# Optimization experiments

Measured on AMD Instinct MI355X. Metric: run time of the kernel, lower is better.

The kernel has to match this reference:

```python
import jax, jax.numpy as jnp
import numpy as np

BLOCK = 64  # block_len

def segsum(x):
    # x: (..., T) -> (..., T, T) lower-triangular segment sums, -inf above diagonal
    T = x.shape[-1]
    cs = jnp.cumsum(x, axis=-1)
    seg = cs[..., :, None] - cs[..., None, :]
    mask = jnp.tril(jnp.ones((T, T), dtype=bool))
    return jnp.where(mask, seg, -jnp.inf)

def setup_inputs() -> dict:
    key = jax.random.key(0)
    k1, k2, k3, k4 = jax.random.split(key, 4)
    b, T, h, p, n = 2, 4096, 32, 64, 64
    X  = jax.random.normal(k1, (b, T, h, p), dtype=jnp.float32)
    # decay rates: negative, bounded, for numerical stability of exp(segsum)
    A  = -0.5 * jax.random.uniform(k2, (b, T, h), dtype=jnp.float32)
    Bm = jax.random.normal(k3, (b, T, h, n), dtype=jnp.float32)
    Cm = jax.random.normal(k4, (b, T, h, n), dtype=jnp.float32)
    return {"X": X, "A": A, "Bm": Bm, "Cm": Cm}

def reference(X, A, Bm, Cm):
    b, T, h, p = X.shape
    n = Bm.shape[-1]
    l = BLOCK
    c = T // l
    # chunk into blocks: b (c l) ... -> b c l ...
    Xb = X.reshape(b, c, l, h, p)
    Bb = Bm.reshape(b, c, l, h, n)
    Cb = Cm.reshape(b, c, l, h, n)
    Ab = A.reshape(b, c, l, h).transpose(0, 3, 1, 2)  # b h c l
    A_cs = jnp.cumsum(Ab, axis=-1)                    # b h c l
    # 1. intra-chunk (diagonal block) output
    L = jnp.exp(segsum(Ab))                           # b h c l l
    Y_diag = jnp.einsum('bclhn,bcshn,bhcls,bcshp->bclhp', Cb, Bb, L, Xb)
    # 2. per-chunk final states
    decay_states = jnp.exp(A_cs[:, :, :, -1:] - A_cs)  # b h c l
    states = jnp.einsum('bclhn,bhcl,bclhp->bchpn', Bb, decay_states, Xb)
    # 3. inter-chunk recurrence (initial state = 0)
    states = jnp.concatenate([jnp.zeros_like(states[:, :1]), states], axis=1)  # b (c+1) h p n
    chunk_sums = jnp.pad(A_cs[:, :, :, -1], ((0, 0), (0, 0), (1, 0)))          # b h (c+1)
    decay_chunk = jnp.exp(segsum(chunk_sums))                                  # b h (c+1) (c+1)
    new_states = jnp.einsum('bhzc,bchpn->bzhpn', decay_chunk, states)[:, :-1]  # b c h p n
    # 4. state -> output (off-diagonal blocks)
    state_decay_out = jnp.exp(A_cs)                                            # b h c l
    Y_off = jnp.einsum('bclhn,bchpn,bhcl->bclhp', Cb, new_states, state_decay_out)
    return (Y_diag + Y_off).reshape(b, T, h, p)
```

## Files before the change

### kernel.cpp

```cpp
#include <hip/hip_runtime.h>
#include <cstddef>

#define NB 2
#define T_ 4096
#define H_ 32
#define P_ 64
#define N_ 64
#define L_ 64
#define C_ 64
#define LDB 72

typedef __attribute__((ext_vector_type(8))) short short8;
typedef __attribute__((ext_vector_type(4))) short short4v;
typedef __attribute__((ext_vector_type(4))) float f32x4;

static __device__ inline short f2bf(float f) {
    unsigned u = __builtin_bit_cast(unsigned, f);
    u += 0x7fffu + ((u >> 16) & 1u);
    return (short)(u >> 16);
}

static __device__ inline short8 ldfrag(const short* s, int t16, int kt, int lane) {
    return *(const short8*)(s + (t16 * 16 + (lane & 15)) * LDB + kt * 32 + ((lane >> 4) * 8));
}

__global__ __launch_bounds__(256) void k1_states(
    const float* __restrict__ X, const float* __restrict__ A,
    const float* __restrict__ Bm, float* __restrict__ St, float* __restrict__ tot)
{
    __shared__ short sXt[L_ * LDB];
    __shared__ short sBt[L_ * LDB];
    __shared__ float sAcs[L_];

    const int tid = threadIdx.x, lane = tid & 63, wv = tid >> 6;
    const int idx = blockIdx.x;
    const int h  = idx & (H_ - 1);
    const int c  = (idx >> 5) & (C_ - 1);
    const int bb = idx >> 11;
    const int t0 = c * L_;

    if (wv == 0) {
        float v = A[(size_t)(bb * T_ + t0 + lane) * H_ + h];
        #pragma unroll
        for (int d = 1; d < 64; d <<= 1) {
            float o = __shfl_up(v, (unsigned)d);
            if (lane >= d) v += o;
        }
        sAcs[lane] = v;
        if (lane == 63) tot[(bb * H_ + h) * C_ + c] = v;
    }
    __syncthreads();
    const float totv = sAcs[L_ - 1];

    const int bi = tid >> 4, bp = tid & 15;
    const int i0 = bi * 4, p0 = bp * 4;
    float4 xr[4], br[4];
    #pragma unroll
    for (int k = 0; k < 4; k++) {
        const size_t g = ((size_t)(bb * T_ + t0 + i0 + k) * H_ + h) * P_ + p0;
        xr[k] = *(const float4*)(X + g);
        br[k] = *(const float4*)(Bm + g);
    }
    float dec[4];
    #pragma unroll
    for (int k = 0; k < 4; k++) dec[k] = expf(totv - sAcs[i0 + k]);
    #pragma unroll
    for (int j = 0; j < 4; j++) {
        short4v vx, vb;
        #pragma unroll
        for (int k = 0; k < 4; k++) {
            vx[k] = f2bf(((const float*)&xr[k])[j]);
            vb[k] = f2bf(((const float*)&br[k])[j] * dec[k]);
        }
        *(short4v*)&sXt[(p0 + j) * LDB + i0] = vx;
        *(short4v*)&sBt[(p0 + j) * LDB + i0] = vb;
    }
    __syncthreads();

    const short8 a0 = ldfrag(sXt, wv, 0, lane);
    const short8 a1 = ldfrag(sXt, wv, 1, lane);
    const size_t sbase = ((size_t)((bb * C_ + c) * H_ + h)) * (N_ * P_);
    const int prow = wv * 16 + (lane >> 4) * 4;
    const int ncol = lane & 15;
    #pragma unroll
    for (int nt = 0; nt < 4; nt++) {
        f32x4 acc = {0.f, 0.f, 0.f, 0.f};
        acc = __builtin_amdgcn_mfma_f32_16x16x32_bf16(a0, ldfrag(sBt, nt, 0, lane), acc, 0, 0, 0);
        acc = __builtin_amdgcn_mfma_f32_16x16x32_bf16(a1, ldfrag(sBt, nt, 1, lane), acc, 0, 0, 0);
        #pragma unroll
        for (int r = 0; r < 4; r++)
            St[sbase + (size_t)(prow + r) * N_ + nt * 16 + ncol] = acc[r];
    }
}

__global__ __launch_bounds__(256) void k2_scan(
    float* __restrict__ St, const float* __restrict__ tot)
{
    const int idx = blockIdx.x;
    const int split = idx & 7;
    const int h  = (idx >> 3) & (H_ - 1);
    const int bb = idx >> 8;
    const int e  = split * 512 + threadIdx.x;
    const float* tp = &tot[(bb * H_ + h) * C_];

    float c0 = 0.f, c1 = 0.f;
    for (int c = 0; c < C_; c++) {
        const float d = expf(tp[c]);
        const size_t base = ((size_t)((bb * C_ + c) * H_ + h)) * (N_ * P_);
        const float t0v = St[base + e];
        const float t1v = St[base + e + 256];
        St[base + e]       = c0;
        St[base + e + 256] = c1;
        c0 = c0 * d + t0v;
        c1 = c1 * d + t1v;
    }
}

__global__ __launch_bounds__(256) void k3_out(
    const float* __restrict__ X, const float* __restrict__ A,
    const float* __restrict__ Bm, const float* __restrict__ Cm,
    const float* __restrict__ St, float* __restrict__ Y)
{
    __shared__ short sC [L_ * LDB];
    __shared__ short sB [L_ * LDB];
    __shared__ short sXt[L_ * LDB];
    __shared__ short sNS[L_ * LDB];
    __shared__ short sS [L_ * LDB];
    __shared__ float sAcs[L_];

    const int tid = threadIdx.x, lane = tid & 63, wv = tid >> 6;
    const int idx = blockIdx.x;
    const int h  = idx & (H_ - 1);
    const int c  = (idx >> 5) & (C_ - 1);
    const int bb = idx >> 11;
    const int t0 = c * L_;
    const size_t sbase = ((size_t)((bb * C_ + c) * H_ + h)) * (N_ * P_);

    if (wv == 0) {
        float v = A[(size_t)(bb * T_ + t0 + lane) * H_ + h];
        #pragma unroll
        for (int d = 1; d < 64; d <<= 1) {
            float o = __shfl_up(v, (unsigned)d);
            if (lane >= d) v += o;
        }
        sAcs[lane] = v;
    }

    #pragma unroll
    for (int f = tid; f < L_ * 16; f += 256) {
        const int row = f >> 4, c4 = (f & 15) << 2;
        const size_t g = ((size_t)(bb * T_ + t0 + row) * H_ + h) * P_ + c4;
        const float4 vc = *(const float4*)(Cm + g);
        const float4 vb = *(const float4*)(Bm + g);
        const float4 vs = *(const float4*)(St + sbase + (size_t)row * N_ + c4);
        short4v c2, b2, s2;
        #pragma unroll
        for (int k = 0; k < 4; k++) {
            c2[k] = f2bf(((const float*)&vc)[k]);
            b2[k] = f2bf(((const float*)&vb)[k]);
            s2[k] = f2bf(((const float*)&vs)[k]);
        }
        *(short4v*)&sC [row * LDB + c4] = c2;
        *(short4v*)&sB [row * LDB + c4] = b2;
        *(short4v*)&sNS[row * LDB + c4] = s2;
    }
    {
        const int bi = tid >> 4, bp = tid & 15;
        const int i0 = bi * 4, p0 = bp * 4;
        float4 xr[4];
        #pragma unroll
        for (int k = 0; k < 4; k++) {
            const size_t g = ((size_t)(bb * T_ + t0 + i0 + k) * H_ + h) * P_ + p0;
            xr[k] = *(const float4*)(X + g);
        }
        #pragma unroll
        for (int j = 0; j < 4; j++) {
            short4v vx;
            #pragma unroll
            for (int k = 0; k < 4; k++) vx[k] = f2bf(((const float*)&xr[k])[j]);
            *(short4v*)&sXt[(p0 + j) * LDB + i0] = vx;
        }
    }
    __syncthreads();

    const short8 c0f = ldfrag(sC, wv, 0, lane);
    const short8 c1f = ldfrag(sC, wv, 1, lane);
    const int rbase = wv * 16 + (lane >> 4) * 4;
    const int col   = lane & 15;

    f32x4 accO[4];
    #pragma unroll
    for (int pt = 0; pt < 4; pt++) {
        f32x4 a = {0.f, 0.f, 0.f, 0.f};
        a = __builtin_amdgcn_mfma_f32_16x16x32_bf16(c0f, ldfrag(sNS, pt, 0, lane), a, 0, 0, 0);
        a = __builtin_amdgcn_mfma_f32_16x16x32_bf16(c1f, ldfrag(sNS, pt, 1, lane), a, 0, 0, 0);
        accO[pt] = a;
    }

    float csr[4];
    #pragma unroll
    for (int r = 0; r < 4; r++) csr[r] = sAcs[rbase + r];
    #pragma unroll
    for (int st = 0; st < 4; st++) {
        f32x4 a = {0.f, 0.f, 0.f, 0.f};
        a = __builtin_amdgcn_mfma_f32_16x16x32_bf16(c0f, ldfrag(sB, st, 0, lane), a, 0, 0, 0);
        a = __builtin_amdgcn_mfma_f32_16x16x32_bf16(c1f, ldfrag(sB, st, 1, lane), a, 0, 0, 0);
        const int scol = st * 16 + col;
        const float ccs = sAcs[scol];
        #pragma unroll
        for (int r = 0; r < 4; r++) {
            const float v = (scol <= rbase + r) ? a[r] * expf(csr[r] - ccs) : 0.f;
            sS[(rbase + r) * LDB + scol] = f2bf(v);
        }
    }

    const short8 s0f = ldfrag(sS, wv, 0, lane);
    const short8 s1f = ldfrag(sS, wv, 1, lane);
    float exr[4];
    #pragma unroll
    for (int r = 0; r < 4; r++) exr[r] = expf(csr[r]);
    #pragma unroll
    for (int pt = 0; pt < 4; pt++) {
        f32x4 a = {0.f, 0.f, 0.f, 0.f};
        a = __builtin_amdgcn_mfma_f32_16x16x32_bf16(s0f, ldfrag(sXt, pt, 0, lane), a, 0, 0, 0);
        a = __builtin_amdgcn_mfma_f32_16x16x32_bf16(s1f, ldfrag(sXt, pt, 1, lane), a, 0, 0, 0);
        #pragma unroll
        for (int r = 0; r < 4; r++) {
            const size_t g = ((size_t)(bb * T_ + t0 + rbase + r) * H_ + h) * P_ + pt * 16 + col;
            Y[g] = a[r] + exr[r] * accO[pt][r];
        }
    }
}

extern "C" void kernel_launch(void* const* d_in, const int* in_sizes, int n_in,
                              void* d_out, int out_size, void* d_ws, size_t ws_size,
                              hipStream_t stream)
{
    const float* X  = (const float*)d_in[0];
    const float* A  = (const float*)d_in[1];
    const float* Bm = (const float*)d_in[2];
    const float* Cm = (const float*)d_in[3];
    float* Y   = (float*)d_out;
    float* St  = (float*)d_ws;
    float* tot = St + (size_t)NB * C_ * H_ * N_ * P_;

    k1_states<<<NB * C_ * H_, 256, 0, stream>>>(X, A, Bm, St, tot);
    k2_scan  <<<NB * H_ * 8, 256, 0, stream>>>(St, tot);
    k3_out   <<<NB * C_ * H_, 256, 0, stream>>>(X, A, Bm, Cm, St, Y);
}
```

Measured before the change: 279.3 us.

## Fuse state, scan and output kernels into one sequential-chunk kernel with register carry

Replaces the three-kernel pipeline (per-chunk states, global scan over chunk states, output) with one kernel per (batch, head, 16-column P slice). Each block walks the 64 chunks in order, keeps the running state in registers, and prefetches the next chunk's inputs into registers while computing the current one. This removes the round-trip of the full state tensor through global memory and two kernel launches. The cost is only 256 blocks of serial 64-step work, which lowers parallelism, and the C·Bᵀ intra-chunk product is now recomputed by each of the four P-slice blocks.

```diff
diff --git a/kernel.cpp b/kernel.cpp
--- a/kernel.cpp
+++ b/kernel.cpp
@@ -24,211 +24,169 @@
     return *(const short8*)(s + (t16 * 16 + (lane & 15)) * LDB + kt * 32 + ((lane >> 4) * 8));
 }
 
-__global__ __launch_bounds__(256) void k1_states(
+__global__ __launch_bounds__(256) void fused_ssd(
     const float* __restrict__ X, const float* __restrict__ A,
-    const float* __restrict__ Bm, float* __restrict__ St, float* __restrict__ tot)
+    const float* __restrict__ Bm, const float* __restrict__ Cm,
+    float* __restrict__ Y)
 {
-    __shared__ short sXt[L_ * LDB];
+    __shared__ short sC [L_ * LDB];
+    __shared__ short sB [L_ * LDB];
     __shared__ short sBt[L_ * LDB];
-    __shared__ float sAcs[L_];
+    __shared__ short sS [L_ * LDB];
+    __shared__ short sXt[16 * LDB];
+    __shared__ short sNS[16 * LDB];
+    __shared__ float sAcs[2][L_];
 
     const int tid = threadIdx.x, lane = tid & 63, wv = tid >> 6;
     const int idx = blockIdx.x;
-    const int h  = idx & (H_ - 1);
-    const int c  = (idx >> 5) & (C_ - 1);
-    const int bb = idx >> 11;
-    const int t0 = c * L_;
-
+    const int q  = idx & 3;
+    const int h  = (idx >> 2) & (H_ - 1);
+    const int bb = idx >> 7;
+    const int p0 = q * 16;
+
+    const int bi = tid >> 4, bp = tid & 15;
+    const int xrow = tid >> 2, xpq = tid & 3;
+
+    float4 rC[4], rB[4], rX;
+    float rA;
+    f32x4 carry = {0.f, 0.f, 0.f, 0.f};
+
+    #pragma unroll
+    for (int k = 0; k < 4; k++) {
+        const size_t g = ((size_t)(bb * T_ + 4 * bi + k) * H_ + h) * P_ + 4 * bp;
+        rC[k] = *(const float4*)(Cm + g);
+        rB[k] = *(const float4*)(Bm + g);
+    }
+    rX = *(const float4*)(X + ((size_t)(bb * T_ + xrow) * H_ + h) * P_ + p0 + 4 * xpq);
+    rA = (tid < 64) ? A[(size_t)(bb * T_ + lane) * H_ + h] : 0.f;
     if (wv == 0) {
-        float v = A[(size_t)(bb * T_ + t0 + lane) * H_ + h];
+        float v = rA;
         #pragma unroll
         for (int d = 1; d < 64; d <<= 1) {
             float o = __shfl_up(v, (unsigned)d);
             if (lane >= d) v += o;
         }
-        sAcs[lane] = v;
-        if (lane == 63) tot[(bb * H_ + h) * C_ + c] = v;
+        sAcs[0][lane] = v;
     }
     __syncthreads();
-    const float totv = sAcs[L_ - 1];
-
-    const int bi = tid >> 4, bp = tid & 15;
-    const int i0 = bi * 4, p0 = bp * 4;
-    float4 xr[4], br[4];
-    #pragma unroll
-    for (int k = 0; k < 4; k++) {
-        const size_t g = ((size_t)(bb * T_ + t0 + i0 + k) * H_ + h) * P_ + p0;
-        xr[k] = *(const float4*)(X + g);
-        br[k] = *(const float4*)(Bm + g);
-    }
-    float dec[4];
-    #pragma unroll
-    for (int k = 0; k < 4; k++) dec[k] = expf(totv - sAcs[i0 + k]);
-    #pragma unroll
-    for (int j = 0; j < 4; j++) {
-        short4v vx, vb;
-        #pragma unroll
-        for (int k = 0; k < 4; k++) {
-            vx[k] = f2bf(((const float*)&xr[k])[j]);
-            vb[k] = f2bf(((const float*)&br[k])[j] * dec[k]);
-        }
-        *(short4v*)&sXt[(p0 + j) * LDB + i0] = vx;
-        *(short4v*)&sBt[(p0 + j) * LDB + i0] = vb;
-    }
-    __syncthreads();
-
-    const short8 a0 = ldfrag(sXt, wv, 0, lane);
-    const short8 a1 = ldfrag(sXt, wv, 1, lane);
-    const size_t sbase = ((size_t)((bb * C_ + c) * H_ + h)) * (N_ * P_);
-    const int prow = wv * 16 + (lane >> 4) * 4;
-    const int ncol = lane & 15;
-    #pragma unroll
-    for (int nt = 0; nt < 4; nt++) {
-        f32x4 acc = {0.f, 0.f, 0.f, 0.f};
-        acc = __builtin_amdgcn_mfma_f32_16x16x32_bf16(a0, ldfrag(sBt, nt, 0, lane), acc, 0, 0, 0);
-        acc = __builtin_amdgcn_mfma_f32_16x16x32_bf16(a1, ldfrag(sBt, nt, 1, lane), acc, 0, 0, 0);
-        #pragma unroll
-        for (int r = 0; r < 4; r++)
-            St[sbase + (size_t)(prow + r) * N_ + nt * 16 + ncol] = acc[r];
-    }
-}
-
-__global__ __launch_bounds__(256) void k2_scan(
-    float* __restrict__ St, const float* __restrict__ tot)
-{
-    const int idx = blockIdx.x;
-    const int split = idx & 7;
-    const int h  = (idx >> 3) & (H_ - 1);
-    const int bb = idx >> 8;
-    const int e  = split * 512 + threadIdx.x;
-    const float* tp = &tot[(bb * H_ + h) * C_];
-
-    float c0 = 0.f, c1 = 0.f;
+
     for (int c = 0; c < C_; c++) {
-        const float d = expf(tp[c]);
-        const size_t base = ((size_t)((bb * C_ + c) * H_ + h)) * (N_ * P_);
-        const float t0v = St[base + e];
-        const float t1v = St[base + e + 256];
-        St[base + e]       = c0;
-        St[base + e + 256] = c1;
-        c0 = c0 * d + t0v;
-        c1 = c1 * d + t1v;
-    }
-}
-
-__global__ __launch_bounds__(256) void k3_out(
-    const float* __restrict__ X, const float* __restrict__ A,
-    const float* __restrict__ Bm, const float* __restrict__ Cm,
-    const float* __restrict__ St, float* __restrict__ Y)
-{
-    __shared__ short sC [L_ * LDB];
-    __shared__ short sB [L_ * LDB];
-    __shared__ short sXt[L_ * LDB];
-    __shared__ short sNS[L_ * LDB];
-    __shared__ short sS [L_ * LDB];
-    __shared__ float sAcs[L_];
-
-    const int tid = threadIdx.x, lane = tid & 63, wv = tid >> 6;
-    const int idx = blockIdx.x;
-    const int h  = idx & (H_ - 1);
-    const int c  = (idx >> 5) & (C_ - 1);
-    const int bb = idx >> 11;
-    const int t0 = c * L_;
-    const size_t sbase = ((size_t)((bb * C_ + c) * H_ + h)) * (N_ * P_);
-
-    if (wv == 0) {
-        float v = A[(size_t)(bb * T_ + t0 + lane) * H_ + h];
-        #pragma unroll
-        for (int d = 1; d < 64; d <<= 1) {
-            float o = __shfl_up(v, (unsigned)d);
-            if (lane >= d) v += o;
-        }
-        sAcs[lane] = v;
-    }
-
-    #pragma unroll
-    for (int f = tid; f < L_ * 16; f += 256) {
-        const int row = f >> 4, c4 = (f & 15) << 2;
-        const size_t g = ((size_t)(bb * T_ + t0 + row) * H_ + h) * P_ + c4;
-        const float4 vc = *(const float4*)(Cm + g);
-        const float4 vb = *(const float4*)(Bm + g);
-        const float4 vs = *(const float4*)(St + sbase + (size_t)row * N_ + c4);
-        short4v c2, b2, s2;
-        #pragma unroll
-        for (int k = 0; k < 4; k++) {
-            c2[k] = f2bf(((const float*)&vc)[k]);
-            b2[k] = f2bf(((const float*)&vb)[k]);
-            s2[k] = f2bf(((const float*)&vs)[k]);
-        }
-        *(short4v*)&sC [row * LDB + c4] = c2;
-        *(short4v*)&sB [row * LDB + c4] = b2;
-        *(short4v*)&sNS[row * LDB + c4] = s2;
-    }
-    {
-        const int bi = tid >> 4, bp = tid & 15;
-        const int i0 = bi * 4, p0 = bp * 4;
-        float4 xr[4];
-        #pragma unroll
-        for (int k = 0; k < 4; k++) {
-            const size_t g = ((size_t)(bb * T_ + t0 + i0 + k) * H_ + h) * P_ + p0;
-            xr[k] = *(const float4*)(X + g);
-        }
-        #pragma unroll
-        for (int j = 0; j < 4; j++) {
-            short4v vx;
-            #pragma unroll
-            for (int k = 0; k < 4; k++) vx[k] = f2bf(((const float*)&xr[k])[j]);
-            *(short4v*)&sXt[(p0 + j) * LDB + i0] = vx;
-        }
-    }
-    __syncthreads();
-
-    const short8 c0f = ldfrag(sC, wv, 0, lane);
-    const short8 c1f = ldfrag(sC, wv, 1, lane);
-    const int rbase = wv * 16 + (lane >> 4) * 4;
-    const int col   = lane & 15;
-
-    f32x4 accO[4];
-    #pragma unroll
-    for (int pt = 0; pt < 4; pt++) {
-        f32x4 a = {0.f, 0.f, 0.f, 0.f};
-        a = __builtin_amdgcn_mfma_f32_16x16x32_bf16(c0f, ldfrag(sNS, pt, 0, lane), a, 0, 0, 0);
-        a = __builtin_amdgcn_mfma_f32_16x16x32_bf16(c1f, ldfrag(sNS, pt, 1, lane), a, 0, 0, 0);
-        accO[pt] = a;
-    }
-
-    float csr[4];
-    #pragma unroll
-    for (int r = 0; r < 4; r++) csr[r] = sAcs[rbase + r];
-    #pragma unroll
-    for (int st = 0; st < 4; st++) {
-        f32x4 a = {0.f, 0.f, 0.f, 0.f};
-        a = __builtin_amdgcn_mfma_f32_16x16x32_bf16(c0f, ldfrag(sB, st, 0, lane), a, 0, 0, 0);
-        a = __builtin_amdgcn_mfma_f32_16x16x32_bf16(c1f, ldfrag(sB, st, 1, lane), a, 0, 0, 0);
-        const int scol = st * 16 + col;
-        const float ccs = sAcs[scol];
+        const int buf = c & 1;
+        const int t0 = c * L_;
+        const float* acs = sAcs[buf];
+
+        {
+            const float totv = acs[L_ - 1];
+            float dec[4];
+            #pragma unroll
+            for (int k = 0; k < 4; k++) dec[k] = expf(totv - acs[4 * bi + k]);
+            #pragma unroll
+            for (int k = 0; k < 4; k++) {
+                short4v vc, vb;
+                #pragma unroll
+                for (int j = 0; j < 4; j++) {
+                    vc[j] = f2bf(((const float*)&rC[k])[j]);
+                    vb[j] = f2bf(((const float*)&rB[k])[j]);
+                }
+                *(short4v*)&sC[(4 * bi + k) * LDB + 4 * bp] = vc;
+                *(short4v*)&sB[(4 * bi + k) * LDB + 4 * bp] = vb;
+            }
+            #pragma unroll
+            for (int j = 0; j < 4; j++) {
+                short4v vt;
+                #pragma unroll
+                for (int k = 0; k < 4; k++)
+                    vt[k] = f2bf(((const float*)&rB[k])[j] * dec[k]);
+                *(short4v*)&sBt[(4 * bp + j) * LDB + 4 * bi] = vt;
+            }
+            #pragma unroll
+            for (int j = 0; j < 4; j++)
+                sXt[(4 * xpq + j) * LDB + xrow] = f2bf(((const float*)&rX)[j]);
+            {
+                const int prow = (lane >> 4) * 4, ncol = wv * 16 + (lane & 15);
+                #pragma unroll
+                for (int r = 0; r < 4; r++)
+                    sNS[(prow + r) * LDB + ncol] = f2bf(carry[r]);
+            }
+        }
+        __syncthreads();
+
+        if (c + 1 < C_) {
+            const int t1 = t0 + L_;
+            #pragma unroll
+            for (int k = 0; k < 4; k++) {
+                const size_t g = ((size_t)(bb * T_ + t1 + 4 * bi + k) * H_ + h) * P_ + 4 * bp;
+                rC[k] = *(const float4*)(Cm + g);
+                rB[k] = *(const float4*)(Bm + g);
+            }
+            rX = *(const float4*)(X + ((size_t)(bb * T_ + t1 + xrow) * H_ + h) * P_ + p0 + 4 * xpq);
+            rA = (tid < 64) ? A[(size_t)(bb * T_ + t1 + lane) * H_ + h] : 0.f;
+        }
+
+        const int rb = (lane >> 4) * 4;
+        const int rbase = wv * 16 + rb;
+        const int col = lane & 15;
+        float csr[4];
+        #pragma unroll
+        for (int r = 0; r < 4; r++) csr[r] = acs[rbase + r];
+        const float totv = acs[L_ - 1];
+
+        const short8 c0f = ldfrag(sC, wv, 0, lane);
+        const short8 c1f = ldfrag(sC, wv, 1, lane);
+
+        f32x4 accY = {0.f, 0.f, 0.f, 0.f};
+        accY = __builtin_amdgcn_mfma_f32_16x16x32_bf16(c0f, ldfrag(sNS, 0, 0, lane), accY, 0, 0, 0);
+        accY = __builtin_amdgcn_mfma_f32_16x16x32_bf16(c1f, ldfrag(sNS, 0, 1, lane), accY, 0, 0, 0);
+        #pragma unroll
+        for (int r = 0; r < 4; r++) accY[r] *= expf(csr[r]);
+
+        #pragma unroll
+        for (int st = 0; st < 4; st++) {
+            f32x4 a = {0.f, 0.f, 0.f, 0.f};
+            a = __builtin_amdgcn_mfma_f32_16x16x32_bf16(c0f, ldfrag(sB, st, 0, lane), a, 0, 0, 0);
+            a = __builtin_amdgcn_mfma_f32_16x16x32_bf16(c1f, ldfrag(sB, st, 1, lane), a, 0, 0, 0);
+            const int scol = st * 16 + col;
+            const float ccs = acs[scol];
+            #pragma unroll
+            for (int r = 0; r < 4; r++) {
+                const float v = (scol <= rbase + r) ? a[r] * expf(csr[r] - ccs) : 0.f;
+                sS[(rbase + r) * LDB + scol] = f2bf(v);
+            }
+        }
+
+        {
+            const short8 s0f = ldfrag(sS, wv, 0, lane);
+            const short8 s1f = ldfrag(sS, wv, 1, lane);
+            accY = __builtin_amdgcn_mfma_f32_16x16x32_bf16(s0f, ldfrag(sXt, 0, 0, lane), accY, 0, 0, 0);
+            accY = __builtin_amdgcn_mfma_f32_16x16x32_bf16(s1f, ldfrag(sXt, 0, 1, lane), accY, 0, 0, 0);
+        }
+
+        {
+            f32x4 stf = {0.f, 0.f, 0.f, 0.f};
+            stf = __builtin_amdgcn_mfma_f32_16x16x32_bf16(ldfrag(sXt, 0, 0, lane), ldfrag(sBt, wv, 0, lane), stf, 0, 0, 0);
+            stf = __builtin_amdgcn_mfma_f32_16x16x32_bf16(ldfrag(sXt, 0, 1, lane), ldfrag(sBt, wv, 1, lane), stf, 0, 0, 0);
+            const float etot = expf(totv);
+            #pragma unroll
+            for (int r = 0; r < 4; r++) carry[r] = carry[r] * etot + stf[r];
+        }
+
+        if (wv == 0 && c + 1 < C_) {
+            float v = rA;
+            #pragma unroll
+            for (int d = 1; d < 64; d <<= 1) {
+                float o = __shfl_up(v, (unsigned)d);
+                if (lane >= d) v += o;
+            }
+            sAcs[buf ^ 1][lane] = v;
+        }
+
         #pragma unroll
         for (int r = 0; r < 4; r++) {
-            const float v = (scol <= rbase + r) ? a[r] * expf(csr[r] - ccs) : 0.f;
-            sS[(rbase + r) * LDB + scol] = f2bf(v);
-        }
-    }
-
-    const short8 s0f = ldfrag(sS, wv, 0, lane);
-    const short8 s1f = ldfrag(sS, wv, 1, lane);
-    float exr[4];
-    #pragma unroll
-    for (int r = 0; r < 4; r++) exr[r] = expf(csr[r]);
-    #pragma unroll
-    for (int pt = 0; pt < 4; pt++) {
-        f32x4 a = {0.f, 0.f, 0.f, 0.f};
-        a = __builtin_amdgcn_mfma_f32_16x16x32_bf16(s0f, ldfrag(sXt, pt, 0, lane), a, 0, 0, 0);
-        a = __builtin_amdgcn_mfma_f32_16x16x32_bf16(s1f, ldfrag(sXt, pt, 1, lane), a, 0, 0, 0);
-        #pragma unroll
-        for (int r = 0; r < 4; r++) {
-            const size_t g = ((size_t)(bb * T_ + t0 + rbase + r) * H_ + h) * P_ + pt * 16 + col;
-            Y[g] = a[r] + exr[r] * accO[pt][r];
-        }
+            const size_t g = ((size_t)(bb * T_ + t0 + rbase + r) * H_ + h) * P_ + p0 + col;
+            Y[g] = accY[r];
+        }
+
+        __syncthreads();
     }
 }
 
@@ -240,11 +198,7 @@
     const float* A  = (const float*)d_in[1];
     const float* Bm = (const float*)d_in[2];
     const float* Cm = (const float*)d_in[3];
-    float* Y   = (float*)d_out;
-    float* St  = (float*)d_ws;
-    float* tot = St + (size_t)NB * C_ * H_ * N_ * P_;
-
-    k1_states<<<NB * C_ * H_, 256, 0, stream>>>(X, A, Bm, St, tot);
-    k2_scan  <<<NB * H_ * 8, 256, 0, stream>>>(St, tot);
-    k3_out   <<<NB * C_ * H_, 256, 0, stream>>>(X, A, Bm, Cm, St, Y);
-}
+    float* Y = (float*)d_out;
+
+    fused_ssd<<<NB * H_ * 4, 256, 0, stream>>>(X, A, Bm, Cm, Y);
+}
```

Result: slower. 316.4 us (+13.3%).
